# Kernel tuning notes

Hardware: AMD Instinct MI355X
Metric: run time of the kernel (lower is better)

The kernel has to match this reference:

```python
import jax, jax.numpy as jnp
import numpy as np

ALPHA = 0.2  # LeakyReLU slope in GAT
OUT_SLOPE = 0.01  # default nn.LeakyyReLU slope for self.out
B, E, IN_DIM, HID, HEADS = 4, 2048, 32, 18, 3
DH = HID // HEADS  # per-head out dim = 6


def _leaky(x, slope):
    return jnp.where(x > 0, x, slope * x)


def _gat_head(x, adj, W, a):
    # x: [B,E,in], W: [in,dh], a: [2*dh,1]
    h = jnp.einsum('bei,id->bed', x, W)                      # [B,E,dh]
    d = h.shape[-1]
    # score[b,i,j] = leakyrelu(a . concat(h_i, h_j)) = leakyrelu(h_i.a1 + h_j.a2)
    e1 = jnp.einsum('bed,d->be', h, a[:d, 0])
    e2 = jnp.einsum('bed,d->be', h, a[d:, 0])
    score = _leaky(e1[:, :, None] + e2[:, None, :], ALPHA)   # [B,E,E]
    scores = jnp.where(adj == 1.0, score, 0.0)
    logits = jnp.where(adj > 0.0, scores, -30.0)
    att = jax.nn.softmax(logits, axis=2)                     # softmax over j
    # h_prime[b,j,d] = sum_i att[b,i,j] * h[b,i,d]  (torch sums over dim=1)
    h_prime = jnp.einsum('bij,bid->bjd', att, h)
    return jax.nn.elu(h_prime)  # concat=True -> elu


def _gat_multihead(x, adj, Ws, As):
    # Ws: [H,in,dh], As: [H,2*dh,1]
    outs = jax.vmap(lambda W, a: _gat_head(x, adj, W, a))(Ws, As)  # [H,B,E,dh]
    H, b, e, d = outs.shape
    return jnp.moveaxis(outs, 0, 2).reshape(b, e, H * d)  # concat heads last-dim


def _gcn(x, adj2d, W, b):
    return adj2d @ (x @ W) + b


def setup_inputs() -> dict:
    key = jax.random.key(0)
    ks = jax.random.split(key, 16)
    node_input = jax.random.normal(ks[0], (B, E, IN_DIM), jnp.float32)
    uv_filed = jax.random.normal(ks[1], (B, E, IN_DIM), jnp.float32)
    adj = jax.random.randint(ks[2], (B, E, E), 0, 2).astype(jnp.float32)
    s = 0.1
    Wt1 = jax.random.normal(ks[3], (HEADS, IN_DIM, DH), jnp.float32) * s
    at1 = jax.random.normal(ks[4], (HEADS, 2 * DH, 1), jnp.float32) * s
    Wt2 = jax.random.normal(ks[5], (HEADS, IN_DIM, DH), jnp.float32) * s
    at2 = jax.random.normal(ks[6], (HEADS, 2 * DH, 1), jnp.float32) * s
    Wg1 = jax.random.normal(ks[7], (HID, 16), jnp.float32) * s
    bg1 = jnp.zeros((16,), jnp.float32)
    Wg2 = jax.random.normal(ks[8], (16, 2), jnp.float32) * s
    bg2 = jnp.zeros((2,), jnp.float32)
    Wo1 = jax.random.normal(ks[9], (HID, 16), jnp.float32) * s
    bo1 = jnp.zeros((16,), jnp.float32)
    Wo2 = jax.random.normal(ks[10], (16, 2), jnp.float32) * s
    bo2 = jnp.zeros((2,), jnp.float32)
    return dict(node_input=node_input, uv_filed=uv_filed, adj=adj,
                Wt1=Wt1, at1=at1, Wt2=Wt2, at2=at2,
                Wg1=Wg1, bg1=bg1, Wg2=Wg2, bg2=bg2,
                Wo1=Wo1, bo1=bo1, Wo2=Wo2, bo2=bo2)


def reference(node_input, uv_filed, adj, Wt1, at1, Wt2, at2,
              Wg1, bg1, Wg2, bg2, Wo1, bo1, Wo2, bo2):
    h = _gat_multihead(node_input, adj, Wt1, at1)  # [B,E,18]
    o = _gat_multihead(uv_filed, adj, Wt2, at2)    # [B,E,18]
    a0 = adj[0]
    Y = jax.nn.relu(_gcn(h[0], a0, Wg1, bg1))
    O = jax.nn.relu(_gcn(o[0], a0, Wo1, bo1))
    Y = _gcn(Y, a0, Wg2, bg2)
    O = _gcn(O, a0, Wo2, bo2)
    return (jax.nn.log_softmax(Y, axis=1), _leaky(O, OUT_SLOPE))
```

## Files before the change

### kernel.cpp

```cpp
#include <hip/hip_runtime.h>
#include <hip/hip_bf16.h>


__global__ __launch_bounds__(256) void k0_bitmask(
    const float* __restrict__ adj0, unsigned int* __restrict__ bm) {
  int lane = threadIdx.x & 63, w = threadIdx.x >> 6;
  int row = blockIdx.x * 4 + w;
  const float* arow = adj0 + (size_t)row * 2048;
#pragma unroll 4
  for (int it = 0; it < 32; ++it) {
    float v = arow[it * 64 + lane];
    unsigned long long mask = __ballot(v == 1.0f);
    if (lane == 0) bm[row * 64 + it * 2] = (unsigned int)mask;
    else if (lane == 32) bm[row * 64 + it * 2 + 1] = (unsigned int)(mask >> 32);
  }
}

__global__ __launch_bounds__(256) void k1_features(
    const float* __restrict__ node, const float* __restrict__ uv,
    const float* __restrict__ Wt1, const float* __restrict__ at1,
    const float* __restrict__ Wt2, const float* __restrict__ at2,
    float* __restrict__ hcol, float* __restrict__ pack1, float* __restrict__ pack2) {
  __shared__ float sW[192];
  __shared__ float sA[12];
  int b = blockIdx.x;
  int g = b / 24;
  int h = (b / 8) % 3;
  int e = (b % 8) * 256 + threadIdx.x;
  const float* W = (g ? Wt2 : Wt1) + h * 192;
  const float* A = (g ? at2 : at1) + h * 12;
  const float* x = (g ? uv : node) + e * 32;
  if (threadIdx.x < 192) sW[threadIdx.x] = W[threadIdx.x];
  if (threadIdx.x < 12) sA[threadIdx.x] = A[threadIdx.x];
  __syncthreads();
  float xv[32];
#pragma unroll
  for (int i = 0; i < 32; ++i) xv[i] = x[i];
  float hv[6];
#pragma unroll
  for (int d = 0; d < 6; ++d) hv[d] = 0.f;
#pragma unroll
  for (int i = 0; i < 32; ++i)
#pragma unroll
    for (int d = 0; d < 6; ++d) hv[d] += xv[i] * sW[i * 6 + d];
  float e1 = 0.f, e2 = 0.f;
#pragma unroll
  for (int d = 0; d < 6; ++d) {
    e1 += hv[d] * sA[d];
    e2 += hv[d] * sA[6 + d];
  }
  int c = g * 3 + h;
#pragma unroll
  for (int d = 0; d < 6; ++d) hcol[(c * 6 + d) * 2048 + e] = hv[d];
  pack1[c * 2048 + e] = e1;
  pack1[(6 + c) * 2048 + e] = __expf(e1);
  pack1[(12 + c) * 2048 + e] = __expf(0.2f * e1);
  pack2[c * 2048 + e] = e2;
  pack2[(6 + c) * 2048 + e] = __expf(e2);
  pack2[(12 + c) * 2048 + e] = __expf(0.2f * e2);
}

__global__ __launch_bounds__(384) void k2_rowsum(
    const unsigned int* __restrict__ bm, const float* __restrict__ pack1,
    const float* __restrict__ pack2, float* __restrict__ invrs) {
  int tid = threadIdx.x;
  int c = tid >> 6, lane = tid & 63;
  int i0 = blockIdx.x * 8;
  const float4* p2_4 = (const float4*)pack2;
  float e1r[8], p1r[8], q1r[8], sum[8];
#pragma unroll
  for (int r = 0; r < 8; ++r) {
    e1r[r] = pack1[c * 2048 + i0 + r];
    p1r[r] = pack1[(6 + c) * 2048 + i0 + r];
    q1r[r] = pack1[(12 + c) * 2048 + i0 + r];
    sum[r] = 0.f;
  }
  int sh = (lane & 7) * 4;
#pragma unroll
  for (int it = 0; it < 8; ++it) {
    int j4 = it * 64 + lane;
    float4 e2 = p2_4[c * 512 + j4];
    float4 p2 = p2_4[(6 + c) * 512 + j4];
    float4 q2 = p2_4[(12 + c) * 512 + j4];
    int wbase = it * 8 + (lane >> 3);
    float abx, aby, abz, abw;
#pragma unroll
    for (int r = 0; r < 8; ++r) {
      unsigned int wd = bm[(i0 + r) * 64 + wbase] >> sh;
      { float e = e1r[r] + e2.x; bool p = e > 0.f;
        abx = (p ? p1r[r] : q1r[r]) * (p ? p2.x : q2.x); }
      { float e = e1r[r] + e2.y; bool p = e > 0.f;
        aby = (p ? p1r[r] : q1r[r]) * (p ? p2.y : q2.y); }
      { float e = e1r[r] + e2.z; bool p = e > 0.f;
        abz = (p ? p1r[r] : q1r[r]) * (p ? p2.z : q2.z); }
      { float e = e1r[r] + e2.w; bool p = e > 0.f;
        abw = (p ? p1r[r] : q1r[r]) * (p ? p2.w : q2.w); }
      float s = ((wd & 1u) ? abx : 0.f) + ((wd & 2u) ? aby : 0.f) +
                ((wd & 4u) ? abz : 0.f) + ((wd & 8u) ? abw : 0.f);
      sum[r] += s;
    }
  }
#pragma unroll
  for (int r = 0; r < 8; ++r) {
#pragma unroll
    for (int off = 32; off > 0; off >>= 1) sum[r] += __shfl_down(sum[r], off);
  }
  if (lane == 0) {
#pragma unroll
    for (int r = 0; r < 8; ++r) invrs[c * 2048 + i0 + r] = 1.0f / sum[r];
  }
}

__global__ __launch_bounds__(384) void k3_hprime(
    const unsigned int* __restrict__ bm, const float* __restrict__ hcol,
    const float* __restrict__ pack1, const float* __restrict__ pack2,
    const float* __restrict__ invrs, float* __restrict__ hp) {
  __shared__ float4 sPack[6 * 64];
  __shared__ float sHS[6 * 64 * 8];
  __shared__ unsigned int sM[64 * 4];
  float4* sHS4 = (float4*)sHS;
  int tid = threadIdx.x;
  int c6 = tid >> 6, jl = tid & 63;
  int j0 = blockIdx.x * 128;
  int i0 = blockIdx.y * 64;
  int jA = j0 + jl, jB = jA + 64;
  float e2A = pack2[c6 * 2048 + jA];
  float p2A = pack2[(6 + c6) * 2048 + jA];
  float q2A = pack2[(12 + c6) * 2048 + jA];
  float e2B = pack2[c6 * 2048 + jB];
  float p2B = pack2[(6 + c6) * 2048 + jB];
  float q2B = pack2[(12 + c6) * 2048 + jB];
  {
    int cc = c6, ii = jl;
    float e1 = pack1[cc * 2048 + i0 + ii];
    float p1 = pack1[(6 + cc) * 2048 + i0 + ii];
    float q1 = pack1[(12 + cc) * 2048 + i0 + ii];
    sPack[cc * 64 + ii] = make_float4(e1, p1, q1, 0.f);
    float iv = invrs[cc * 2048 + i0 + ii];
#pragma unroll
    for (int d = 0; d < 6; ++d)
      sHS[(cc * 64 + ii) * 8 + d] = hcol[(cc * 6 + d) * 2048 + i0 + ii] * iv;
    sHS[(cc * 64 + ii) * 8 + 6] = 0.f;
    sHS[(cc * 64 + ii) * 8 + 7] = 0.f;
  }
  if (tid < 256) sM[tid] = bm[(size_t)(i0 + (tid >> 2)) * 64 + (j0 >> 5) + (tid & 3)];
  __syncthreads();
  float aA0 = 0.f, aA1 = 0.f, aA2 = 0.f, aA3 = 0.f, aA4 = 0.f, aA5 = 0.f;
  float aB0 = 0.f, aB1 = 0.f, aB2 = 0.f, aB3 = 0.f, aB4 = 0.f, aB5 = 0.f;
  int hi = jl >> 5;
  int shj = jl & 31;
#pragma unroll 8
  for (int ii = 0; ii < 64; ++ii) {
    float4 pk = sPack[c6 * 64 + ii];
    float4 h0 = sHS4[(c6 * 64 + ii) * 2];
    float4 h1 = sHS4[(c6 * 64 + ii) * 2 + 1];
    unsigned int wdA = sM[ii * 4 + hi];
    unsigned int wdB = sM[ii * 4 + 2 + hi];
    {
      float e = pk.x + e2A; bool p = e > 0.f;
      float ab = (p ? pk.y : pk.z) * (p ? p2A : q2A);
      float wgt = ((wdA >> shj) & 1u) ? ab : 0.f;
      aA0 += wgt * h0.x; aA1 += wgt * h0.y; aA2 += wgt * h0.z;
      aA3 += wgt * h0.w; aA4 += wgt * h1.x; aA5 += wgt * h1.y;
    }
    {
      float e = pk.x + e2B; bool p = e > 0.f;
      float ab = (p ? pk.y : pk.z) * (p ? p2B : q2B);
      float wgt = ((wdB >> shj) & 1u) ? ab : 0.f;
      aB0 += wgt * h0.x; aB1 += wgt * h0.y; aB2 += wgt * h0.z;
      aB3 += wgt * h0.w; aB4 += wgt * h1.x; aB5 += wgt * h1.y;
    }
  }
  int kb = c6 * 6;
  atomicAdd(&hp[(kb + 0) * 2048 + jA], aA0);
  atomicAdd(&hp[(kb + 1) * 2048 + jA], aA1);
  atomicAdd(&hp[(kb + 2) * 2048 + jA], aA2);
  atomicAdd(&hp[(kb + 3) * 2048 + jA], aA3);
  atomicAdd(&hp[(kb + 4) * 2048 + jA], aA4);
  atomicAdd(&hp[(kb + 5) * 2048 + jA], aA5);
  atomicAdd(&hp[(kb + 0) * 2048 + jB], aB0);
  atomicAdd(&hp[(kb + 1) * 2048 + jB], aB1);
  atomicAdd(&hp[(kb + 2) * 2048 + jB], aB2);
  atomicAdd(&hp[(kb + 3) * 2048 + jB], aB3);
  atomicAdd(&hp[(kb + 4) * 2048 + jB], aB4);
  atomicAdd(&hp[(kb + 5) * 2048 + jB], aB5);
}

__global__ __launch_bounds__(256) void k4_T(
    const float* __restrict__ hp, const float* __restrict__ Wg1,
    const float* __restrict__ Wo1, float* __restrict__ T) {
  __shared__ float sHP[32 * 37];
  __shared__ float sWg[288], sWo[288];
  int tid = threadIdx.x;
  int j0 = blockIdx.x * 32;
  for (int idx = tid; idx < 288; idx += 256) {
    sWg[idx] = Wg1[idx];
    sWo[idx] = Wo1[idx];
  }
  for (int idx = tid; idx < 1152; idx += 256) {
    int r = idx >> 5, jl = idx & 31;
    sHP[jl * 37 + r] = hp[r * 2048 + j0 + jl];
  }
  __syncthreads();
  int jl = tid & 31, wq = tid >> 5;
  int gat = wq >> 2;
  int c0 = (wq & 3) * 4;
  const float* Wp = gat ? sWo : sWg;
  float acc[4];
#pragma unroll
  for (int t = 0; t < 4; ++t) acc[t] = 0.f;
#pragma unroll
  for (int r = 0; r < 18; ++r) {
    float x = sHP[jl * 37 + gat * 18 + r];
    float hc = x > 0.f ? x : __expf(x) - 1.f;
#pragma unroll
    for (int t = 0; t < 4; ++t) acc[t] += hc * Wp[r * 16 + c0 + t];
  }
#pragma unroll
  for (int t = 0; t < 4; ++t) T[(j0 + jl) * 32 + gat * 16 + c0 + t] = acc[t];
}

__global__ __launch_bounds__(256) void k5_gcn1(
    const unsigned int* __restrict__ bm, const float* __restrict__ T,
    float* __restrict__ Craw) {
  __shared__ unsigned int sM[64 * 4];
  __shared__ float4 sT4[128 * 8];
  const float4* T4 = (const float4*)T;
  int tid = threadIdx.x;
  int rl = tid & 31, cg = tid >> 5;
  int i0 = blockIdx.x * 64;
  int k0 = blockIdx.y * 128;
  if (tid < 256) sM[tid] = bm[(size_t)(i0 + (tid >> 2)) * 64 + (k0 >> 5) + (tid & 3)];
  for (int idx = tid; idx < 1024; idx += 256) sT4[idx] = T4[k0 * 8 + idx];
  __syncthreads();
  float a0x = 0.f, a0y = 0.f, a0z = 0.f, a0w = 0.f;
  float a1x = 0.f, a1y = 0.f, a1z = 0.f, a1w = 0.f;
#pragma unroll
  for (int wi = 0; wi < 4; ++wi) {
    unsigned int wA = sM[rl * 4 + wi];
    unsigned int wB = sM[(rl + 32) * 4 + wi];
#pragma unroll 16
    for (int kb = 0; kb < 32; ++kb) {
      float4 t = sT4[(wi * 32 + kb) * 8 + cg];
      float mA = (float)((wA >> kb) & 1u);
      float mB = (float)((wB >> kb) & 1u);
      a0x += mA * t.x; a0y += mA * t.y; a0z += mA * t.z; a0w += mA * t.w;
      a1x += mB * t.x; a1y += mB * t.y; a1z += mB * t.z; a1w += mB * t.w;
    }
  }
  float* d0 = &Craw[(i0 + rl) * 32 + cg * 4];
  atomicAdd(d0 + 0, a0x); atomicAdd(d0 + 1, a0y);
  atomicAdd(d0 + 2, a0z); atomicAdd(d0 + 3, a0w);
  float* d1 = &Craw[(i0 + rl + 32) * 32 + cg * 4];
  atomicAdd(d1 + 0, a1x); atomicAdd(d1 + 1, a1y);
  atomicAdd(d1 + 2, a1z); atomicAdd(d1 + 3, a1w);
}

__global__ __launch_bounds__(256) void k6_T2(
    const float* __restrict__ Craw, const float* __restrict__ bg1,
    const float* __restrict__ Wg2, const float* __restrict__ bo1,
    const float* __restrict__ Wo2, float* __restrict__ T2) {
  int tid = threadIdx.x;
  int wave = tid >> 6, lane = tid & 63;
  int j = blockIdx.x * 8 + wave * 2 + (lane >> 5);
  int cl = lane & 31;
  int gat = cl >> 4, cc = cl & 15;
  float x = Craw[j * 32 + cl];
  x += gat ? bo1[cc] : bg1[cc];
  x = x > 0.f ? x : 0.f;
  float wa = gat ? Wo2[cc * 2 + 0] : Wg2[cc * 2 + 0];
  float wb = gat ? Wo2[cc * 2 + 1] : Wg2[cc * 2 + 1];
  float pa = x * wa, pb = x * wb;
#pragma unroll
  for (int m = 8; m > 0; m >>= 1) {
    pa += __shfl_xor(pa, m);
    pb += __shfl_xor(pb, m);
  }
  if (cc == 0) {
    T2[j * 4 + gat * 2 + 0] = pa;
    T2[j * 4 + gat * 2 + 1] = pb;
  }
}

__global__ __launch_bounds__(256) void k7_final(
    const unsigned int* __restrict__ bm, const float* __restrict__ T2,
    const float* __restrict__ bg2, const float* __restrict__ bo2,
    float* __restrict__ out) {
  int tid = threadIdx.x;
  int lane = tid & 63, w = tid >> 6;
  int r = blockIdx.x * 4 + w;
  const float4* T24 = (const float4*)T2;
  float4 acc = make_float4(0.f, 0.f, 0.f, 0.f);
  int sh = lane & 31;
#pragma unroll 8
  for (int it = 0; it < 32; ++it) {
    int k = it * 64 + lane;
    unsigned int wd = bm[r * 64 + it * 2 + (lane >> 5)];
    float m = (float)((wd >> sh) & 1u);
    float4 t = T24[k];
    acc.x += m * t.x;
    acc.y += m * t.y;
    acc.z += m * t.z;
    acc.w += m * t.w;
  }
#pragma unroll
  for (int off = 32; off > 0; off >>= 1) {
    acc.x += __shfl_down(acc.x, off);
    acc.y += __shfl_down(acc.y, off);
    acc.z += __shfl_down(acc.z, off);
    acc.w += __shfl_down(acc.w, off);
  }
  if (lane == 0) {
    float y0 = acc.x + bg2[0], y1 = acc.y + bg2[1];
    float m = fmaxf(y0, y1);
    float ls = m + logf(__expf(y0 - m) + __expf(y1 - m));
    out[r * 2 + 0] = y0 - ls;
    out[r * 2 + 1] = y1 - ls;
    float o0 = acc.z + bo2[0], o1 = acc.w + bo2[1];
    out[4096 + r * 2 + 0] = o0 > 0.f ? o0 : 0.01f * o0;
    out[4096 + r * 2 + 1] = o1 > 0.f ? o1 : 0.01f * o1;
  }
}

extern "C" void kernel_launch(void* const* d_in, const int* in_sizes, int n_in,
                              void* d_out, int out_size, void* d_ws, size_t ws_size,
                              hipStream_t stream) {
  const float* node = (const float*)d_in[0];
  const float* uv = (const float*)d_in[1];
  const float* adj = (const float*)d_in[2];
  const float* Wt1 = (const float*)d_in[3];
  const float* at1 = (const float*)d_in[4];
  const float* Wt2 = (const float*)d_in[5];
  const float* at2 = (const float*)d_in[6];
  const float* Wg1 = (const float*)d_in[7];
  const float* bg1 = (const float*)d_in[8];
  const float* Wg2 = (const float*)d_in[9];
  const float* bg2 = (const float*)d_in[10];
  const float* Wo1 = (const float*)d_in[11];
  const float* bo1 = (const float*)d_in[12];
  const float* Wo2 = (const float*)d_in[13];
  const float* bo2 = (const float*)d_in[14];
  float* ws = (float*)d_ws;
  float* hcol = ws;
  float* pack1 = ws + 73728;
  float* pack2 = ws + 110592;
  float* invrs = ws + 147456;
  float* T = ws + 159744;
  float* T2 = ws + 225280;
  float* hp = ws + 233472;
  float* Craw = ws + 307200;
  unsigned int* bm = (unsigned int*)(ws + 372736);
  float* out = (float*)d_out;

  hipMemsetAsync(hp, 0, (73728 + 65536) * sizeof(float), stream);
  k0_bitmask<<<512, 256, 0, stream>>>(adj, bm);
  k1_features<<<48, 256, 0, stream>>>(node, uv, Wt1, at1, Wt2, at2, hcol, pack1, pack2);
  k2_rowsum<<<256, 384, 0, stream>>>(bm, pack1, pack2, invrs);
  k3_hprime<<<dim3(16, 32), 384, 0, stream>>>(bm, hcol, pack1, pack2, invrs, hp);
  k4_T<<<64, 256, 0, stream>>>(hp, Wg1, Wo1, T);
  k5_gcn1<<<dim3(32, 16), 256, 0, stream>>>(bm, T, Craw);
  k6_T2<<<256, 256, 0, stream>>>(Craw, bg1, Wg2, bo1, Wo2, T2);
  k7_final<<<512, 256, 0, stream>>>(bm, T2, bg2, bo2, out);
}
```

Measured before the change: 212.2 us.

## Replace atomic split-K accumulation with partial buffers reduced in consumer kernels

```diff
diff --git a/kernel.cpp b/kernel.cpp
--- a/kernel.cpp
+++ b/kernel.cpp
@@ -114,7 +114,7 @@
 __global__ __launch_bounds__(384) void k3_hprime(
     const unsigned int* __restrict__ bm, const float* __restrict__ hcol,
     const float* __restrict__ pack1, const float* __restrict__ pack2,
-    const float* __restrict__ invrs, float* __restrict__ hp) {
+    const float* __restrict__ invrs, float* __restrict__ hp_part) {
   __shared__ float4 sPack[6 * 64];
   __shared__ float sHS[6 * 64 * 8];
   __shared__ unsigned int sM[64 * 4];
@@ -122,7 +122,6 @@
   int tid = threadIdx.x;
   int c6 = tid >> 6, jl = tid & 63;
   int j0 = blockIdx.x * 128;
-  int i0 = blockIdx.y * 64;
   int jA = j0 + jl, jB = jA + 64;
   float e2A = pack2[c6 * 2048 + jA];
   float p2A = pack2[(6 + c6) * 2048 + jA];
@@ -130,99 +129,106 @@
   float e2B = pack2[c6 * 2048 + jB];
   float p2B = pack2[(6 + c6) * 2048 + jB];
   float q2B = pack2[(12 + c6) * 2048 + jB];
-  {
-    int cc = c6, ii = jl;
-    float e1 = pack1[cc * 2048 + i0 + ii];
-    float p1 = pack1[(6 + cc) * 2048 + i0 + ii];
-    float q1 = pack1[(12 + cc) * 2048 + i0 + ii];
-    sPack[cc * 64 + ii] = make_float4(e1, p1, q1, 0.f);
-    float iv = invrs[cc * 2048 + i0 + ii];
-#pragma unroll
-    for (int d = 0; d < 6; ++d)
-      sHS[(cc * 64 + ii) * 8 + d] = hcol[(cc * 6 + d) * 2048 + i0 + ii] * iv;
-    sHS[(cc * 64 + ii) * 8 + 6] = 0.f;
-    sHS[(cc * 64 + ii) * 8 + 7] = 0.f;
-  }
-  if (tid < 256) sM[tid] = bm[(size_t)(i0 + (tid >> 2)) * 64 + (j0 >> 5) + (tid & 3)];
-  __syncthreads();
   float aA0 = 0.f, aA1 = 0.f, aA2 = 0.f, aA3 = 0.f, aA4 = 0.f, aA5 = 0.f;
   float aB0 = 0.f, aB1 = 0.f, aB2 = 0.f, aB3 = 0.f, aB4 = 0.f, aB5 = 0.f;
   int hi = jl >> 5;
   int shj = jl & 31;
+  int ibeg = blockIdx.y * 128;
+  for (int i0 = ibeg; i0 < ibeg + 128; i0 += 64) {
+    __syncthreads();
+    {
+      int cc = c6, ii = jl;
+      float e1 = pack1[cc * 2048 + i0 + ii];
+      float p1 = pack1[(6 + cc) * 2048 + i0 + ii];
+      float q1 = pack1[(12 + cc) * 2048 + i0 + ii];
+      sPack[cc * 64 + ii] = make_float4(e1, p1, q1, 0.f);
+      float iv = invrs[cc * 2048 + i0 + ii];
+#pragma unroll
+      for (int d = 0; d < 6; ++d)
+        sHS[(cc * 64 + ii) * 8 + d] = hcol[(cc * 6 + d) * 2048 + i0 + ii] * iv;
+      sHS[(cc * 64 + ii) * 8 + 6] = 0.f;
+      sHS[(cc * 64 + ii) * 8 + 7] = 0.f;
+    }
+    if (tid < 256) sM[tid] = bm[(size_t)(i0 + (tid >> 2)) * 64 + (j0 >> 5) + (tid & 3)];
+    __syncthreads();
 #pragma unroll 8
-  for (int ii = 0; ii < 64; ++ii) {
-    float4 pk = sPack[c6 * 64 + ii];
-    float4 h0 = sHS4[(c6 * 64 + ii) * 2];
-    float4 h1 = sHS4[(c6 * 64 + ii) * 2 + 1];
-    unsigned int wdA = sM[ii * 4 + hi];
-    unsigned int wdB = sM[ii * 4 + 2 + hi];
-    {
-      float e = pk.x + e2A; bool p = e > 0.f;
-      float ab = (p ? pk.y : pk.z) * (p ? p2A : q2A);
-      float wgt = ((wdA >> shj) & 1u) ? ab : 0.f;
-      aA0 += wgt * h0.x; aA1 += wgt * h0.y; aA2 += wgt * h0.z;
-      aA3 += wgt * h0.w; aA4 += wgt * h1.x; aA5 += wgt * h1.y;
+    for (int ii = 0; ii < 64; ++ii) {
+      float4 pk = sPack[c6 * 64 + ii];
+      float4 h0 = sHS4[(c6 * 64 + ii) * 2];
+      float4 h1 = sHS4[(c6 * 64 + ii) * 2 + 1];
+      unsigned int wdA = sM[ii * 4 + hi];
+      unsigned int wdB = sM[ii * 4 + 2 + hi];
+      {
+        float e = pk.x + e2A; bool p = e > 0.f;
+        float ab = (p ? pk.y : pk.z) * (p ? p2A : q2A);
+        float wgt = ((wdA >> shj) & 1u) ? ab : 0.f;
+        aA0 += wgt * h0.x; aA1 += wgt * h0.y; aA2 += wgt * h0.z;
+        aA3 += wgt * h0.w; aA4 += wgt * h1.x; aA5 += wgt * h1.y;
+      }
+      {
+        float e = pk.x + e2B; bool p = e > 0.f;
+        float ab = (p ? pk.y : pk.z) * (p ? p2B : q2B);
+        float wgt = ((wdB >> shj) & 1u) ? ab : 0.f;
+        aB0 += wgt * h0.x; aB1 += wgt * h0.y; aB2 += wgt * h0.z;
+        aB3 += wgt * h0.w; aB4 += wgt * h1.x; aB5 += wgt * h1.y;
+      }
     }
-    {
-      float e = pk.x + e2B; bool p = e > 0.f;
-      float ab = (p ? pk.y : pk.z) * (p ? p2B : q2B);
-      float wgt = ((wdB >> shj) & 1u) ? ab : 0.f;
-      aB0 += wgt * h0.x; aB1 += wgt * h0.y; aB2 += wgt * h0.z;
-      aB3 += wgt * h0.w; aB4 += wgt * h1.x; aB5 += wgt * h1.y;
-    }
-  }
+  }
+  float* hp = hp_part + (size_t)blockIdx.y * 73728;
   int kb = c6 * 6;
-  atomicAdd(&hp[(kb + 0) * 2048 + jA], aA0);
-  atomicAdd(&hp[(kb + 1) * 2048 + jA], aA1);
-  atomicAdd(&hp[(kb + 2) * 2048 + jA], aA2);
-  atomicAdd(&hp[(kb + 3) * 2048 + jA], aA3);
-  atomicAdd(&hp[(kb + 4) * 2048 + jA], aA4);
-  atomicAdd(&hp[(kb + 5) * 2048 + jA], aA5);
-  atomicAdd(&hp[(kb + 0) * 2048 + jB], aB0);
-  atomicAdd(&hp[(kb + 1) * 2048 + jB], aB1);
-  atomicAdd(&hp[(kb + 2) * 2048 + jB], aB2);
-  atomicAdd(&hp[(kb + 3) * 2048 + jB], aB3);
-  atomicAdd(&hp[(kb + 4) * 2048 + jB], aB4);
-  atomicAdd(&hp[(kb + 5) * 2048 + jB], aB5);
+  hp[(kb + 0) * 2048 + jA] = aA0;
+  hp[(kb + 1) * 2048 + jA] = aA1;
+  hp[(kb + 2) * 2048 + jA] = aA2;
+  hp[(kb + 3) * 2048 + jA] = aA3;
+  hp[(kb + 4) * 2048 + jA] = aA4;
+  hp[(kb + 5) * 2048 + jA] = aA5;
+  hp[(kb + 0) * 2048 + jB] = aB0;
+  hp[(kb + 1) * 2048 + jB] = aB1;
+  hp[(kb + 2) * 2048 + jB] = aB2;
+  hp[(kb + 3) * 2048 + jB] = aB3;
+  hp[(kb + 4) * 2048 + jB] = aB4;
+  hp[(kb + 5) * 2048 + jB] = aB5;
 }
 
 __global__ __launch_bounds__(256) void k4_T(
-    const float* __restrict__ hp, const float* __restrict__ Wg1,
+    const float* __restrict__ hp_part, const float* __restrict__ Wg1,
     const float* __restrict__ Wo1, float* __restrict__ T) {
-  __shared__ float sHP[32 * 37];
+  __shared__ float sHP[16 * 37];
   __shared__ float sWg[288], sWo[288];
   int tid = threadIdx.x;
-  int j0 = blockIdx.x * 32;
+  int j0 = blockIdx.x * 16;
   for (int idx = tid; idx < 288; idx += 256) {
     sWg[idx] = Wg1[idx];
     sWo[idx] = Wo1[idx];
   }
-  for (int idx = tid; idx < 1152; idx += 256) {
-    int r = idx >> 5, jl = idx & 31;
-    sHP[jl * 37 + r] = hp[r * 2048 + j0 + jl];
+  for (int idx = tid; idx < 576; idx += 256) {
+    int r = idx >> 4, jl = idx & 15;
+    float s = 0.f;
+#pragma unroll
+    for (int sp = 0; sp < 16; ++sp)
+      s += hp_part[(size_t)sp * 73728 + r * 2048 + j0 + jl];
+    sHP[jl * 37 + r] = s;
   }
   __syncthreads();
-  int jl = tid & 31, wq = tid >> 5;
-  int gat = wq >> 2;
-  int c0 = (wq & 3) * 4;
+  int jl = tid & 15, wq = tid >> 4;
+  int gat = wq >> 3;
+  int c0 = (wq & 7) * 2;
   const float* Wp = gat ? sWo : sWg;
-  float acc[4];
-#pragma unroll
-  for (int t = 0; t < 4; ++t) acc[t] = 0.f;
+  float a0 = 0.f, a1 = 0.f;
 #pragma unroll
   for (int r = 0; r < 18; ++r) {
     float x = sHP[jl * 37 + gat * 18 + r];
     float hc = x > 0.f ? x : __expf(x) - 1.f;
-#pragma unroll
-    for (int t = 0; t < 4; ++t) acc[t] += hc * Wp[r * 16 + c0 + t];
-  }
-#pragma unroll
-  for (int t = 0; t < 4; ++t) T[(j0 + jl) * 32 + gat * 16 + c0 + t] = acc[t];
+    a0 += hc * Wp[r * 16 + c0];
+    a1 += hc * Wp[r * 16 + c0 + 1];
+  }
+  T[(j0 + jl) * 32 + gat * 16 + c0] = a0;
+  T[(j0 + jl) * 32 + gat * 16 + c0 + 1] = a1;
 }
 
 __global__ __launch_bounds__(256) void k5_gcn1(
     const unsigned int* __restrict__ bm, const float* __restrict__ T,
-    float* __restrict__ Craw) {
+    float* __restrict__ Craw_part) {
   __shared__ unsigned int sM[64 * 4];
   __shared__ float4 sT4[128 * 8];
   const float4* T4 = (const float4*)T;
@@ -248,16 +254,13 @@
       a1x += mB * t.x; a1y += mB * t.y; a1z += mB * t.z; a1w += mB * t.w;
     }
   }
-  float* d0 = &Craw[(i0 + rl) * 32 + cg * 4];
-  atomicAdd(d0 + 0, a0x); atomicAdd(d0 + 1, a0y);
-  atomicAdd(d0 + 2, a0z); atomicAdd(d0 + 3, a0w);
-  float* d1 = &Craw[(i0 + rl + 32) * 32 + cg * 4];
-  atomicAdd(d1 + 0, a1x); atomicAdd(d1 + 1, a1y);
-  atomicAdd(d1 + 2, a1z); atomicAdd(d1 + 3, a1w);
+  float* base = Craw_part + (size_t)blockIdx.y * 65536;
+  *(float4*)&base[(i0 + rl) * 32 + cg * 4] = make_float4(a0x, a0y, a0z, a0w);
+  *(float4*)&base[(i0 + rl + 32) * 32 + cg * 4] = make_float4(a1x, a1y, a1z, a1w);
 }
 
 __global__ __launch_bounds__(256) void k6_T2(
-    const float* __restrict__ Craw, const float* __restrict__ bg1,
+    const float* __restrict__ Craw_part, const float* __restrict__ bg1,
     const float* __restrict__ Wg2, const float* __restrict__ bo1,
     const float* __restrict__ Wo2, float* __restrict__ T2) {
   int tid = threadIdx.x;
@@ -265,7 +268,9 @@
   int j = blockIdx.x * 8 + wave * 2 + (lane >> 5);
   int cl = lane & 31;
   int gat = cl >> 4, cc = cl & 15;
-  float x = Craw[j * 32 + cl];
+  float x = 0.f;
+#pragma unroll
+  for (int sp = 0; sp < 16; ++sp) x += Craw_part[(size_t)sp * 65536 + j * 32 + cl];
   x += gat ? bo1[cc] : bg1[cc];
   x = x > 0.f ? x : 0.f;
   float wa = gat ? Wo2[cc * 2 + 0] : Wg2[cc * 2 + 0];
@@ -347,18 +352,17 @@
   float* invrs = ws + 147456;
   float* T = ws + 159744;
   float* T2 = ws + 225280;
-  float* hp = ws + 233472;
-  float* Craw = ws + 307200;
-  unsigned int* bm = (unsigned int*)(ws + 372736);
+  unsigned int* bm = (unsigned int*)(ws + 233472);
+  float* hp_part = ws + 364544;
+  float* Craw_part = ws + 1544192;
   float* out = (float*)d_out;
 
-  hipMemsetAsync(hp, 0, (73728 + 65536) * sizeof(float), stream);
   k0_bitmask<<<512, 256, 0, stream>>>(adj, bm);
   k1_features<<<48, 256, 0, stream>>>(node, uv, Wt1, at1, Wt2, at2, hcol, pack1, pack2);
   k2_rowsum<<<256, 384, 0, stream>>>(bm, pack1, pack2, invrs);
-  k3_hprime<<<dim3(16, 32), 384, 0, stream>>>(bm, hcol, pack1, pack2, invrs, hp);
-  k4_T<<<64, 256, 0, stream>>>(hp, Wg1, Wo1, T);
-  k5_gcn1<<<dim3(32, 16), 256, 0, stream>>>(bm, T, Craw);
-  k6_T2<<<256, 256, 0, stream>>>(Craw, bg1, Wg2, bo1, Wo2, T2);
+  k3_hprime<<<dim3(16, 16), 384, 0, stream>>>(bm, hcol, pack1, pack2, invrs, hp_part);
+  k4_T<<<128, 256, 0, stream>>>(hp_part, Wg1, Wo1, T);
+  k5_gcn1<<<dim3(32, 16), 256, 0, stream>>>(bm, T, Craw_part);
+  k6_T2<<<256, 256, 0, stream>>>(Craw_part, bg1, Wg2, bo1, Wo2, T2);
   k7_final<<<512, 256, 0, stream>>>(bm, T2, bg2, bo2, out);
 }
```

Measured after the change: 183.6 us. -13.4%, faster.
